# Optimization experiments

Hardware: AMD Instinct MI355X
Metric: run time of the kernel (lower is better)

The kernel has to match this reference:

```python
import jax, jax.numpy as jnp
import numpy as np

N_SRC = 1_000_000
N_OUT = 65_536
D = 64

def setup_inputs() -> dict:
    key = jax.random.key(0)
    k1, k2, k3 = jax.random.split(key, 3)
    input = jax.random.normal(k1, (N_OUT, D), dtype=jnp.float32)
    index = jax.random.randint(k2, (N_SRC, D), 0, N_OUT, dtype=jnp.int64)
    src = jax.random.normal(k3, (N_SRC, D), dtype=jnp.float32)
    return {"input": input, "index": index, "src": src}

def reference(input, index, src):
    # torch.scatter_reduce(input, 0, index, src, reduce='sum', include_self=True):
    #   out = input.copy(); out[index[i, j], j] += src[i, j]
    cols = jnp.arange(src.shape[1])[None, :]  # [1, D] broadcasts against index [N, D]
    return input.at[index, cols].add(src)
```

## Files before the change

### kernel.cpp

```cpp
#include <hip/hip_runtime.h>


typedef unsigned int u32;
typedef unsigned short u16;
typedef unsigned long long u64;

#define NBKT 256
#define NBLK 1024
#define BLK  512
#define BATCH 4096
#define CAPR 320
#define CAPS 46
#define CPAD 48
#define FU   16
#define TILE 16384
#define OMAX 130048

#define BAR() asm volatile("s_waitcnt lgkmcnt(0)\n\ts_barrier" ::: "memory")

__global__ void Zero_kernel(u32* p, int n) {
    int i = threadIdx.x;
    if (i < n) p[i] = 0;
}

__global__ void InitOut_kernel(const float4* __restrict__ in, float4* __restrict__ out, int n4) {
    int i = blockIdx.x * blockDim.x + threadIdx.x;
    if (i < n4) out[i] = in[i];
}

__global__ void FallbackAdd_kernel(const int4* __restrict__ index4,
                                   const float4* __restrict__ src4,
                                   float* __restrict__ out, int n4) {
    const int stride = gridDim.x * blockDim.x;
    for (int i = blockIdx.x * blockDim.x + threadIdx.x; i < n4; i += stride) {
        int4 idx = index4[i];
        float4 v = src4[i];
        int jbase = (i & 15) << 2;
        atomicAdd(&out[(idx.x << 6) + jbase + 0], v.x);
        atomicAdd(&out[(idx.y << 6) + jbase + 1], v.y);
        atomicAdd(&out[(idx.z << 6) + jbase + 2], v.z);
        atomicAdd(&out[(idx.w << 6) + jbase + 3], v.w);
    }
}

__global__ __launch_bounds__(BLK) void Scatter_kernel(
        const int* __restrict__ index, const float* __restrict__ src,
        float* __restrict__ val, u16* __restrict__ dst, u16* __restrict__ cntg,
        u32* __restrict__ ocnt, u64* __restrict__ olist,
        int epb, long long E)
{
    __shared__ float sv[NBKT][CPAD];
    __shared__ u16  sd[NBKT][CPAD];
    __shared__ u32  cnt[NBKT];
    __shared__ u32  fltot[NBKT];
    const int t = threadIdx.x;
    const int k = blockIdx.x;
    long long c0 = (long long)k * epb;
    long long c1 = c0 + epb; if (c1 > E) c1 = E;
    if (c0 >= c1) {
        if (t < NBKT) cntg[(size_t)k * NBKT + t] = 0;
        return;
    }
    if (t < NBKT) { cnt[t] = 0; fltot[t] = 0; }
    __syncthreads();

    const int col0 = (t << 3) & 63;
    const size_t rbase = (size_t)k * CAPR;

#define PROC(rr, vv, cc) { \
    int bb = (rr) >> 8; \
    u32 p = atomicAdd(&cnt[bb], 1u); \
    u16 dd = (u16)((((rr) & 255) << 6) | (cc)); \
    if (p < CAPS) { sv[bb][p] = (vv); sd[bb][p] = dd; } \
    else { u32 q = fltot[bb] + p; \
        if (q < CAPR) { size_t pos = (size_t)bb * (NBLK * CAPR) + rbase + q; \
                        val[pos] = (vv); dst[pos] = dd; } \
        else { u32 oi = atomicAdd(ocnt, 1u); \
               if (oi < OMAX) olist[oi] = ((u64)__float_as_uint(vv) << 32) | (u32)(((rr) << 6) + (cc)); } } }

    long long e = c0 + t * 8;
    bool have = e < c1;
    int4 ra, rb; float4 va, vb;
    if (have) {
        ra = *(const int4*)(index + e);     rb = *(const int4*)(index + e + 4);
        va = *(const float4*)(src + e);     vb = *(const float4*)(src + e + 4);
    }

    const int g = t >> 3, lr = t & 7;

    for (long long eb = c0; eb < c1; eb += BATCH) {
        long long en = e + BATCH;
        bool haveN = en < c1;
        int4 rna, rnb; float4 vna, vnb;
        if (haveN) {
            rna = *(const int4*)(index + en);   rnb = *(const int4*)(index + en + 4);
            vna = *(const float4*)(src + en);   vnb = *(const float4*)(src + en + 4);
        }
        if (have) {
            PROC(ra.x, va.x, col0 + 0);
            PROC(ra.y, va.y, col0 + 1);
            PROC(ra.z, va.z, col0 + 2);
            PROC(ra.w, va.w, col0 + 3);
            PROC(rb.x, vb.x, col0 + 4);
            PROC(rb.y, vb.y, col0 + 5);
            PROC(rb.z, vb.z, col0 + 6);
            PROC(rb.w, vb.w, col0 + 7);
        }
        BAR();
        #pragma unroll
        for (int pass = 0; pass < 4; ++pass) {
            int b = (pass << 6) + g;
            u32 c = cnt[b];
            u32 fl = fltot[b];
            if (c > CAPS) {
                for (u32 i = lr; i < CAPS; i += 8) {
                    u32 q = fl + i;
                    if (q < CAPR) {
                        size_t pos = (size_t)b * (NBLK * CAPR) + rbase + q;
                        val[pos] = sv[b][i]; dst[pos] = sd[b][i];
                    } else {
                        u32 oi = atomicAdd(ocnt, 1u);
                        if (oi < OMAX)
                            olist[oi] = ((u64)__float_as_uint(sv[b][i]) << 32) |
                                        (u32)(((u32)b << 14) | sd[b][i]);
                    }
                }
                u32 tot = fl + c;
                u32 pad = ((tot + FU - 1) & ~(FU - 1u)) - tot;
                for (u32 i = lr; i < pad; i += 8) {
                    u32 q = tot + i;
                    if (q < CAPR) {
                        size_t pos = (size_t)b * (NBLK * CAPR) + rbase + q;
                        val[pos] = 0.f; dst[pos] = 0;
                    }
                }
                if (lr == 0) { fltot[b] = tot + pad; cnt[b] = 0; }
            } else {
                u32 fcopy = (c >= FU) ? (c & ~(FU - 1u)) : 0u;
                if (fcopy) {
                    for (u32 u = 0; u < fcopy; u += FU) {
                        u32 s = u + 2 * lr;
                        u32 q = fl + s;
                        if (q + 1 < CAPR) {
                            float2 v2 = *(const float2*)&sv[b][s];
                            u32 d2 = *(const u32*)&sd[b][s];
                            size_t pos = (size_t)b * (NBLK * CAPR) + rbase + q;
                            *(float2*)&val[pos] = v2;
                            *(u32*)&dst[pos] = d2;
                        } else {
                            for (int jj = 0; jj < 2; ++jj) {
                                u32 oi = atomicAdd(ocnt, 1u);
                                if (oi < OMAX)
                                    olist[oi] = ((u64)__float_as_uint(sv[b][s + jj]) << 32) |
                                                (u32)(((u32)b << 14) | sd[b][s + jj]);
                            }
                        }
                    }
                    u32 rem = c - fcopy;
                    for (u32 i = lr; i < rem; i += 8) {
                        sv[b][i] = sv[b][fcopy + i];
                        sd[b][i] = sd[b][fcopy + i];
                    }
                    if (lr == 0) { fltot[b] = fl + fcopy; cnt[b] = rem; }
                }
            }
        }
        BAR();
        ra = rna; rb = rnb; va = vna; vb = vnb; have = haveN; e = en;
    }

    #pragma unroll
    for (int pass = 0; pass < 4; ++pass) {
        int b = (pass << 6) + g;
        u32 c = cnt[b]; if (c > CAPS) c = CAPS;
        u32 fl = fltot[b];
        for (u32 i = lr; i < c; i += 8) {
            u32 q = fl + i;
            if (q < CAPR) {
                size_t pos = (size_t)b * (NBLK * CAPR) + rbase + q;
                val[pos] = sv[b][i]; dst[pos] = sd[b][i];
            } else {
                u32 oi = atomicAdd(ocnt, 1u);
                if (oi < OMAX)
                    olist[oi] = ((u64)__float_as_uint(sv[b][i]) << 32) |
                                (u32)(((u32)b << 14) | sd[b][i]);
            }
        }
    }
    BAR();
    if (t < NBKT) {
        u32 total = fltot[t] + cnt[t];
        if (total > CAPR) total = CAPR;
        cntg[(size_t)k * NBKT + t] = (u16)total;
    }
#undef PROC
}

__global__ __launch_bounds__(1024) void Reduce_kernel(
        const float* __restrict__ val, const u16* __restrict__ dst,
        const u16* __restrict__ cntg, const u32* __restrict__ ocnt,
        const u64* __restrict__ olist, float* __restrict__ out)
{
    __shared__ float tile[TILE];
    const int b = blockIdx.x >> 1;
    const int p = blockIdx.x & 1;
    const int t = threadIdx.x;
    float4* t4 = (float4*)tile;
    for (int i = t; i < TILE / 4; i += 1024) t4[i] = make_float4(0.f, 0.f, 0.f, 0.f);
    BAR();
    const int g = t >> 3, lr = t & 7;
    const size_t bb = (size_t)b * ((size_t)NBLK * CAPR);
    for (int k = p * (NBLK / 2) + g; k < (p + 1) * (NBLK / 2); k += 128) {
        u32 n = cntg[(size_t)k * NBKT + b]; if (n > CAPR) n = CAPR;
        const float* vp = val + bb + (size_t)k * CAPR;
        const u16*  dp = dst + bb + (size_t)k * CAPR;
        u32 n4 = n & ~3u;
        u32 i = (u32)lr * 4;
        if (i < n4) {
            float4 v = *(const float4*)(vp + i);
            ushort4 d = *(const ushort4*)(dp + i);
            for (;;) {
                u32 j = i + 32;
                bool more = j < n4;
                float4 v2; ushort4 d2;
                if (more) {
                    v2 = *(const float4*)(vp + j);
                    d2 = *(const ushort4*)(dp + j);
                }
                atomicAdd(&tile[d.x], v.x);
                atomicAdd(&tile[d.y], v.y);
                atomicAdd(&tile[d.z], v.z);
                atomicAdd(&tile[d.w], v.w);
                if (!more) break;
                v = v2; d = d2; i = j;
            }
        }
        u32 rem = n - n4;
        if ((u32)lr < rem)
            atomicAdd(&tile[dp[n4 + lr]], vp[n4 + lr]);
    }
    if (p == 0) {
        u32 on = *ocnt; if (on > OMAX) on = OMAX;
        for (u32 i = t; i < on; i += 1024) {
            u64 pr = olist[i];
            u32 d = (u32)pr;
            if ((d >> 14) == (u32)b)
                atomicAdd(&tile[d & (TILE - 1)], __uint_as_float((u32)(pr >> 32)));
        }
    }
    BAR();
    float* ob = out + (size_t)b * TILE;
    for (int i = t; i < TILE; i += 1024)
        atomicAdd(&ob[i], tile[i]);
}

extern "C" void kernel_launch(void* const* d_in, const int* in_sizes, int n_in,
                              void* d_out, int out_size, void* d_ws, size_t ws_size,
                              hipStream_t stream) {
    const float* input = (const float*)d_in[0];
    const int*   index = (const int*)d_in[1];
    const float* src   = (const float*)d_in[2];
    float* out = (float*)d_out;
    long long E = (long long)in_sizes[2];

    const size_t off_olist = 64;
    const size_t off_cnt   = off_olist + (size_t)OMAX * 8;
    const size_t off_val   = (size_t)2u << 20;
    const size_t off_dst   = off_val + (size_t)NBKT * NBLK * CAPR * 4;
    const size_t need      = off_dst + (size_t)NBKT * NBLK * CAPR * 2;

    int epb = (int)(((E + NBLK - 1) / NBLK + 63) & ~63LL);

    int n4o = out_size / 4;
    if (ws_size < need || (E & 7) || out_size != NBKT * TILE || epb > 65536) {
        InitOut_kernel<<<(n4o + 255) / 256, 256, 0, stream>>>(
            (const float4*)input, (float4*)out, n4o);
        FallbackAdd_kernel<<<2048, 256, 0, stream>>>(
            (const int4*)index, (const float4*)src, out, (int)(E / 4));
        return;
    }

    char* ws = (char*)d_ws;
    u32*  ocnt  = (u32*)ws;
    u64*  olist = (u64*)(ws + off_olist);
    u16*  cntg  = (u16*)(ws + off_cnt);
    float* val  = (float*)(ws + off_val);
    u16*  dst   = (u16*)(ws + off_dst);

    Zero_kernel<<<1, 64, 0, stream>>>(ocnt, 16);
    InitOut_kernel<<<(n4o + 255) / 256, 256, 0, stream>>>(
        (const float4*)input, (float4*)out, n4o);

    Scatter_kernel<<<NBLK, BLK, 0, stream>>>(index, src, val, dst, cntg,
                                             ocnt, olist, epb, E);
    Reduce_kernel<<<NBKT * 2, 1024, 0, stream>>>(val, dst, cntg, ocnt, olist, out);
}
```

Before: 608.7 us.

## Fuse output init into reduce kernel and use one block per bucket

Drops the separate InitOut kernel. Each reduce block now owns a whole bucket, handling all source chunks and the overflow list, then writes input+tile straight to the output with plain float4 stores instead of global atomics. The manual software prefetch in the inner loop becomes a simple strided loop. This saves one launch, a full pass over the output and the global atomics, but halves the reduce grid to 256 blocks, which lowers parallelism in the atomic-heavy phase.

```diff
diff --git a/kernel.cpp b/kernel.cpp
--- a/kernel.cpp
+++ b/kernel.cpp
@@ -199,47 +199,34 @@
 __global__ __launch_bounds__(1024) void Reduce_kernel(
         const float* __restrict__ val, const u16* __restrict__ dst,
         const u16* __restrict__ cntg, const u32* __restrict__ ocnt,
-        const u64* __restrict__ olist, float* __restrict__ out)
+        const u64* __restrict__ olist,
+        const float* __restrict__ input, float* __restrict__ out)
 {
     __shared__ float tile[TILE];
-    const int b = blockIdx.x >> 1;
-    const int p = blockIdx.x & 1;
-    const int t = threadIdx.x;
+    const int b = blockIdx.x, t = threadIdx.x;
     float4* t4 = (float4*)tile;
     for (int i = t; i < TILE / 4; i += 1024) t4[i] = make_float4(0.f, 0.f, 0.f, 0.f);
-    BAR();
+    __syncthreads();
     const int g = t >> 3, lr = t & 7;
     const size_t bb = (size_t)b * ((size_t)NBLK * CAPR);
-    for (int k = p * (NBLK / 2) + g; k < (p + 1) * (NBLK / 2); k += 128) {
+    for (int k = g; k < NBLK; k += 128) {
         u32 n = cntg[(size_t)k * NBKT + b]; if (n > CAPR) n = CAPR;
         const float* vp = val + bb + (size_t)k * CAPR;
         const u16*  dp = dst + bb + (size_t)k * CAPR;
         u32 n4 = n & ~3u;
-        u32 i = (u32)lr * 4;
-        if (i < n4) {
+        for (u32 i = (u32)lr * 4; i < n4; i += 32) {
             float4 v = *(const float4*)(vp + i);
             ushort4 d = *(const ushort4*)(dp + i);
-            for (;;) {
-                u32 j = i + 32;
-                bool more = j < n4;
-                float4 v2; ushort4 d2;
-                if (more) {
-                    v2 = *(const float4*)(vp + j);
-                    d2 = *(const ushort4*)(dp + j);
-                }
-                atomicAdd(&tile[d.x], v.x);
-                atomicAdd(&tile[d.y], v.y);
-                atomicAdd(&tile[d.z], v.z);
-                atomicAdd(&tile[d.w], v.w);
-                if (!more) break;
-                v = v2; d = d2; i = j;
-            }
+            atomicAdd(&tile[d.x], v.x);
+            atomicAdd(&tile[d.y], v.y);
+            atomicAdd(&tile[d.z], v.z);
+            atomicAdd(&tile[d.w], v.w);
         }
         u32 rem = n - n4;
         if ((u32)lr < rem)
             atomicAdd(&tile[dp[n4 + lr]], vp[n4 + lr]);
     }
-    if (p == 0) {
+    {
         u32 on = *ocnt; if (on > OMAX) on = OMAX;
         for (u32 i = t; i < on; i += 1024) {
             u64 pr = olist[i];
@@ -248,10 +235,14 @@
                 atomicAdd(&tile[d & (TILE - 1)], __uint_as_float((u32)(pr >> 32)));
         }
     }
-    BAR();
-    float* ob = out + (size_t)b * TILE;
-    for (int i = t; i < TILE; i += 1024)
-        atomicAdd(&ob[i], tile[i]);
+    __syncthreads();
+    const float4* in4 = (const float4*)(input + (size_t)b * TILE);
+    float4* o4 = (float4*)(out + (size_t)b * TILE);
+    for (int i = t; i < TILE / 4; i += 1024) {
+        float4 a = in4[i], s = t4[i];
+        a.x += s.x; a.y += s.y; a.z += s.z; a.w += s.w;
+        o4[i] = a;
+    }
 }
 
 extern "C" void kernel_launch(void* const* d_in, const int* in_sizes, int n_in,
@@ -288,10 +279,8 @@
     u16*  dst   = (u16*)(ws + off_dst);
 
     Zero_kernel<<<1, 64, 0, stream>>>(ocnt, 16);
-    InitOut_kernel<<<(n4o + 255) / 256, 256, 0, stream>>>(
-        (const float4*)input, (float4*)out, n4o);
 
     Scatter_kernel<<<NBLK, BLK, 0, stream>>>(index, src, val, dst, cntg,
                                              ocnt, olist, epb, E);
-    Reduce_kernel<<<NBKT * 2, 1024, 0, stream>>>(val, dst, cntg, ocnt, olist, out);
-}
+    Reduce_kernel<<<NBKT, 1024, 0, stream>>>(val, dst, cntg, ocnt, olist, input, out);
+}
```

Result: no change. 597.5 us, median of 2 (-1.8%).
